# Kernel optimization log

Hardware: AMD Instinct MI355X
Metric: run time of the kernel (lower is better)

Reference implementation:

```python
import jax, jax.numpy as jnp
import numpy as np

B, S, E = 8, 2048, 1024
H, DK = 128, 8  # embed_dim = H * DK; DK = n_wires per quantum head


def setup_inputs() -> dict:
    key = jax.random.key(0)
    k1, k2, k3, k4 = jax.random.split(key, 4)
    x = jax.random.normal(k1, (B, S, E), dtype=jnp.float32)
    theta = jax.random.normal(k2, (H, DK), dtype=jnp.float32)  # trainable RX angles per head/wire
    W = jax.random.normal(k3, (E, E), dtype=jnp.float32) * (1.0 / np.sqrt(E))
    b = jax.random.normal(k4, (E,), dtype=jnp.float32) * 0.01
    return {"x": x, "theta": theta, "W": W, "b": b}


def reference(x, theta, W, b):
    # Quantum circuit per token/head: RX(x_i) then RX(theta_i) on wire i starting
    # from |0...0>. Single-qubit RX gates compose: RX(a)RX(b)=RX(a+b), and
    # <Z> after RX(angle)|0> = cos(angle). So the MeasureAll(PauliZ) output is
    # cos(x_i + theta_i) elementwise -- fully vectorized over batch/seq/head/wire.
    Bx, Sx, Ex = x.shape
    Hx, dk = theta.shape
    xs = x.reshape(Bx, Sx, Hx, dk)            # [B,S,H,dk]
    head_out = jnp.cos(xs + theta[None, None])  # [B,S,H,dk]
    out = head_out.reshape(Bx, Sx, Ex)
    return out @ W.T + b                       # combine Linear
```

## Files before the change

kernel.cpp:

```cpp
#include <hip/hip_runtime.h>
#include <hip/hip_bf16.h>
#include <stdint.h>

#define M_DIM 16384
#define N_DIM 1024
#define K_DIM 1024

typedef __attribute__((ext_vector_type(8))) short short8;
typedef __attribute__((ext_vector_type(4))) float f32x4;

#define GLD_LDS(g, l) __builtin_amdgcn_global_load_lds( \
    (const __attribute__((address_space(1))) unsigned int*)(g), \
    (__attribute__((address_space(3))) unsigned int*)(l), 16, 0, 0)

__device__ __forceinline__ unsigned short f2bf(float f) {
  union { float f; unsigned int u; } v;
  v.f = f;
  unsigned int u = v.u + 0x7FFFu + ((v.u >> 16) & 1u);
  return (unsigned short)(u >> 16);
}

#define PREP_A_BLOCKS (M_DIM * K_DIM / (256 * 8))
#define PREP_W_BLOCKS (N_DIM * K_DIM / (256 * 8))
__global__ __launch_bounds__(256) void prep_all(const float* __restrict__ x,
                                                const float* __restrict__ theta,
                                                const float* __restrict__ W,
                                                unsigned short* __restrict__ A,
                                                unsigned short* __restrict__ Wb) {
  if (blockIdx.x < PREP_A_BLOCKS) {
    const long i = ((long)blockIdx.x * 256 + threadIdx.x) * 8;
    const int k = (int)(i & (K_DIM - 1));
    float4 x0 = *(const float4*)(x + i);
    float4 x1 = *(const float4*)(x + i + 4);
    float4 t0 = *(const float4*)(theta + k);
    float4 t1 = *(const float4*)(theta + k + 4);
    union { unsigned short s[8]; short8 v; } o;
    o.s[0] = f2bf(__cosf(x0.x + t0.x));
    o.s[1] = f2bf(__cosf(x0.y + t0.y));
    o.s[2] = f2bf(__cosf(x0.z + t0.z));
    o.s[3] = f2bf(__cosf(x0.w + t0.w));
    o.s[4] = f2bf(__cosf(x1.x + t1.x));
    o.s[5] = f2bf(__cosf(x1.y + t1.y));
    o.s[6] = f2bf(__cosf(x1.z + t1.z));
    o.s[7] = f2bf(__cosf(x1.w + t1.w));
    *(short8*)(A + i) = o.v;
  } else {
    const long i = ((long)(blockIdx.x - PREP_A_BLOCKS) * 256 + threadIdx.x) * 8;
    float4 w0 = *(const float4*)(W + i);
    float4 w1 = *(const float4*)(W + i + 4);
    union { unsigned short s[8]; short8 v; } o;
    o.s[0] = f2bf(w0.x); o.s[1] = f2bf(w0.y); o.s[2] = f2bf(w0.z); o.s[3] = f2bf(w0.w);
    o.s[4] = f2bf(w1.x); o.s[5] = f2bf(w1.y); o.s[6] = f2bf(w1.z); o.s[7] = f2bf(w1.w);
    *(short8*)(Wb + i) = o.v;
  }
}

__global__ __launch_bounds__(512, 2) void gemm_bt(const unsigned short* __restrict__ A,
                                                  const unsigned short* __restrict__ Bt,
                                                  const float* __restrict__ bias,
                                                  float* __restrict__ C) {
  constexpr int BM = 256, BN = 256, BK = 64;
  constexpr int NT = K_DIM / BK;
  __shared__ unsigned short As[2 * BM * BK];
  __shared__ unsigned short Bs[2 * BN * BK];
  const int tid = threadIdx.x;

  const int L = blockIdx.y * 4 + blockIdx.x;
  const int xcd = L & 7;
  const int idx = L >> 3;
  const int by = xcd * 8 + (idx >> 2);
  const int bx = idx & 3;
  const int m0 = by * BM;
  const int n0 = bx * BN;

  const int lane = tid & 63;
  const int wave = tid >> 6;
  const int wm = (wave >> 2) * 128;
  const int wn = (wave & 3) * 64;
  const int fr = lane & 15;
  const int fq = lane >> 4;

  f32x4 acc[8][4] = {};

  const int csw = (tid & 7) ^ ((tid >> 3) & 7);
  const unsigned short* Ag = A + (long)(m0 + (tid >> 3)) * K_DIM + csw * 8;
  const unsigned short* Bg = Bt + (long)(n0 + (tid >> 3)) * K_DIM + csw * 8;
  unsigned short* Asd = As + tid * 8;
  unsigned short* Bsd = Bs + tid * 8;

#pragma unroll
  for (int i = 0; i < 4; ++i) GLD_LDS(Ag + (long)i * 64 * K_DIM, Asd + i * 4096);
#pragma unroll
  for (int i = 0; i < 4; ++i) GLD_LDS(Bg + (long)i * 64 * K_DIM, Bsd + i * 4096);
  Ag += BK;
  Bg += BK;

  for (int t = 0; t < NT; ++t) {
    const int cur = t & 1;
    if (t < NT - 1) {
      unsigned short* Ad = Asd + (cur ^ 1) * (BM * BK);
      unsigned short* Bd = Bsd + (cur ^ 1) * (BN * BK);
#pragma unroll
      for (int i = 0; i < 4; ++i) GLD_LDS(Ag + (long)i * 64 * K_DIM, Ad + i * 4096);
#pragma unroll
      for (int i = 0; i < 4; ++i) GLD_LDS(Bg + (long)i * 64 * K_DIM, Bd + i * 4096);
      Ag += BK;
      Bg += BK;
      asm volatile("s_waitcnt vmcnt(8)" ::: "memory");
    } else {
      asm volatile("s_waitcnt vmcnt(0)" ::: "memory");
    }
    __builtin_amdgcn_s_barrier();
    asm volatile("" ::: "memory");

    const unsigned short* SA = As + cur * (BM * BK);
    const unsigned short* SB = Bs + cur * (BN * BK);
#pragma unroll
    for (int ks = 0; ks < 2; ++ks) {
      const int swz = (((ks * 4 + fq) ^ (lane & 7)) * 8);
      short8 af[8], bf[4];
#pragma unroll
      for (int j = 0; j < 4; ++j)
        bf[j] = *(const short8*)(SB + (wn + j * 16 + fr) * BK + swz);
#pragma unroll
      for (int i = 0; i < 8; ++i)
        af[i] = *(const short8*)(SA + (wm + i * 16 + fr) * BK + swz);
      __builtin_amdgcn_s_setprio(1);
#pragma unroll
      for (int i = 0; i < 8; ++i)
#pragma unroll
        for (int j = 0; j < 4; ++j)
          acc[i][j] = __builtin_amdgcn_mfma_f32_16x16x32_bf16(af[i], bf[j], acc[i][j], 0, 0, 0);
      __builtin_amdgcn_s_setprio(0);
      if (ks == 0) {
        asm volatile("" ::: "memory");
        __builtin_amdgcn_s_barrier();
        asm volatile("" ::: "memory");
      }
    }
    asm volatile("" ::: "memory");
    __builtin_amdgcn_s_barrier();
    asm volatile("" ::: "memory");
  }

  const int cn = lane & 15;
  const int rq = (lane >> 4) * 4;
#pragma unroll
  for (int j = 0; j < 4; ++j) {
    const int n = n0 + wn + j * 16 + cn;
    const float bv = bias[n];
#pragma unroll
    for (int i = 0; i < 8; ++i) {
      const long mb = (long)(m0 + wm + i * 16 + rq) * N_DIM + n;
#pragma unroll
      for (int r = 0; r < 4; ++r)
        C[mb + (long)r * N_DIM] = acc[i][j][r] + bv;
    }
  }
}

extern "C" void kernel_launch(void* const* d_in, const int* in_sizes, int n_in,
                              void* d_out, int out_size, void* d_ws, size_t ws_size,
                              hipStream_t stream) {
  const float* x = (const float*)d_in[0];
  const float* theta = (const float*)d_in[1];
  const float* W = (const float*)d_in[2];
  const float* b = (const float*)d_in[3];
  float* out = (float*)d_out;

  unsigned short* Abf = (unsigned short*)d_ws;
  unsigned short* Wbf = Abf + (size_t)M_DIM * K_DIM;

  hipLaunchKernelGGL(prep_all, dim3(PREP_A_BLOCKS + PREP_W_BLOCKS), dim3(256), 0,
                     stream, x, theta, W, Abf, Wbf);
  hipLaunchKernelGGL(gemm_bt, dim3(N_DIM / 256, M_DIM / 256), dim3(512), 0, stream,
                     Abf, Wbf, b, out);
}
```

Baseline: 152.5 us.

## Restructure GEMM main loop into four-unit half-K LDS pipeline with phased MFMA

```diff
diff --git a/kernel.cpp b/kernel.cpp
--- a/kernel.cpp
+++ b/kernel.cpp
@@ -59,10 +59,9 @@
                                                   const unsigned short* __restrict__ Bt,
                                                   const float* __restrict__ bias,
                                                   float* __restrict__ C) {
-  constexpr int BM = 256, BN = 256, BK = 64;
-  constexpr int NT = K_DIM / BK;
-  __shared__ unsigned short As[2 * BM * BK];
-  __shared__ unsigned short Bs[2 * BN * BK];
+  constexpr int NTT = K_DIM / 64;
+  __shared__ unsigned short As[4 * 8192];
+  __shared__ unsigned short Bs[4 * 8192];
   const int tid = threadIdx.x;
 
   const int L = blockIdx.y * 4 + blockIdx.x;
@@ -70,8 +69,8 @@
   const int idx = L >> 3;
   const int by = xcd * 8 + (idx >> 2);
   const int bx = idx & 3;
-  const int m0 = by * BM;
-  const int n0 = bx * BN;
+  const int m0 = by * 256;
+  const int n0 = bx * 256;
 
   const int lane = tid & 63;
   const int wave = tid >> 6;
@@ -82,65 +81,123 @@
 
   f32x4 acc[8][4] = {};
 
-  const int csw = (tid & 7) ^ ((tid >> 3) & 7);
-  const unsigned short* Ag = A + (long)(m0 + (tid >> 3)) * K_DIM + csw * 8;
-  const unsigned short* Bg = Bt + (long)(n0 + (tid >> 3)) * K_DIM + csw * 8;
-  unsigned short* Asd = As + tid * 8;
-  unsigned short* Bsd = Bs + tid * 8;
-
-#pragma unroll
-  for (int i = 0; i < 4; ++i) GLD_LDS(Ag + (long)i * 64 * K_DIM, Asd + i * 4096);
-#pragma unroll
-  for (int i = 0; i < 4; ++i) GLD_LDS(Bg + (long)i * 64 * K_DIM, Bsd + i * 4096);
-  Ag += BK;
-  Bg += BK;
-
-  for (int t = 0; t < NT; ++t) {
-    const int cur = t & 1;
-    if (t < NT - 1) {
-      unsigned short* Ad = Asd + (cur ^ 1) * (BM * BK);
-      unsigned short* Bd = Bsd + (cur ^ 1) * (BN * BK);
-#pragma unroll
-      for (int i = 0; i < 4; ++i) GLD_LDS(Ag + (long)i * 64 * K_DIM, Ad + i * 4096);
-#pragma unroll
-      for (int i = 0; i < 4; ++i) GLD_LDS(Bg + (long)i * 64 * K_DIM, Bd + i * 4096);
-      Ag += BK;
-      Bg += BK;
-      asm volatile("s_waitcnt vmcnt(8)" ::: "memory");
-    } else {
-      asm volatile("s_waitcnt vmcnt(0)" ::: "memory");
-    }
-    __builtin_amdgcn_s_barrier();
-    asm volatile("" ::: "memory");
-
-    const unsigned short* SA = As + cur * (BM * BK);
-    const unsigned short* SB = Bs + cur * (BN * BK);
-#pragma unroll
-    for (int ks = 0; ks < 2; ++ks) {
-      const int swz = (((ks * 4 + fq) ^ (lane & 7)) * 8);
-      short8 af[8], bf[4];
-#pragma unroll
-      for (int j = 0; j < 4; ++j)
-        bf[j] = *(const short8*)(SB + (wn + j * 16 + fr) * BK + swz);
-#pragma unroll
-      for (int i = 0; i < 8; ++i)
-        af[i] = *(const short8*)(SA + (wm + i * 16 + fr) * BK + swz);
-      __builtin_amdgcn_s_setprio(1);
-#pragma unroll
-      for (int i = 0; i < 8; ++i)
-#pragma unroll
-        for (int j = 0; j < 4; ++j)
-          acc[i][j] = __builtin_amdgcn_mfma_f32_16x16x32_bf16(af[i], bf[j], acc[i][j], 0, 0, 0);
-      __builtin_amdgcn_s_setprio(0);
-      if (ks == 0) {
-        asm volatile("" ::: "memory");
-        __builtin_amdgcn_s_barrier();
-        asm volatile("" ::: "memory");
-      }
-    }
-    asm volatile("" ::: "memory");
-    __builtin_amdgcn_s_barrier();
-    asm volatile("" ::: "memory");
+  const int srow = ((tid >> 5) << 3) | (tid & 7);
+  const int kc = (tid >> 3) & 3;
+  const unsigned short* AgU = A + (long)(m0 + srow) * K_DIM + kc * 8;
+  const unsigned short* BgU = Bt + (long)(n0 + srow) * K_DIM + kc * 8;
+  unsigned short* AsD = As + tid * 8;
+  unsigned short* BsD = Bs + tid * 8;
+
+#define STAGE_A(UNIT, TAU, KH) do { \
+    const unsigned short* g_ = AgU + (TAU) * 64 + (KH) * 32; \
+    unsigned short* d_ = AsD + (UNIT) * 8192; \
+    GLD_LDS(g_, d_); \
+    GLD_LDS(g_ + (long)128 * K_DIM, d_ + 4096); \
+  } while (0)
+#define STAGE_B(UNIT, TAU, KH) do { \
+    const unsigned short* g_ = BgU + (TAU) * 64 + (KH) * 32; \
+    unsigned short* d_ = BsD + (UNIT) * 8192; \
+    GLD_LDS(g_, d_); \
+    GLD_LDS(g_ + (long)128 * K_DIM, d_ + 4096); \
+  } while (0)
+
+  const int baseA = ((wm >> 3) + (fr >> 3)) * 256 + fq * 64 + (fr & 7) * 8;
+  const int baseB = ((wn >> 3) + (fr >> 3)) * 256 + fq * 64 + (fr & 7) * 8;
+
+  short8 bf0, bf1, bf2, bf3;
+
+#define MFMA16(IH, A0, A1, A2, A3) do { \
+    __builtin_amdgcn_s_setprio(1); \
+    acc[(IH)*4+0][0] = __builtin_amdgcn_mfma_f32_16x16x32_bf16(A0, bf0, acc[(IH)*4+0][0], 0, 0, 0); \
+    acc[(IH)*4+0][1] = __builtin_amdgcn_mfma_f32_16x16x32_bf16(A0, bf1, acc[(IH)*4+0][1], 0, 0, 0); \
+    acc[(IH)*4+0][2] = __builtin_amdgcn_mfma_f32_16x16x32_bf16(A0, bf2, acc[(IH)*4+0][2], 0, 0, 0); \
+    acc[(IH)*4+0][3] = __builtin_amdgcn_mfma_f32_16x16x32_bf16(A0, bf3, acc[(IH)*4+0][3], 0, 0, 0); \
+    acc[(IH)*4+1][0] = __builtin_amdgcn_mfma_f32_16x16x32_bf16(A1, bf0, acc[(IH)*4+1][0], 0, 0, 0); \
+    acc[(IH)*4+1][1] = __builtin_amdgcn_mfma_f32_16x16x32_bf16(A1, bf1, acc[(IH)*4+1][1], 0, 0, 0); \
+    acc[(IH)*4+1][2] = __builtin_amdgcn_mfma_f32_16x16x32_bf16(A1, bf2, acc[(IH)*4+1][2], 0, 0, 0); \
+    acc[(IH)*4+1][3] = __builtin_amdgcn_mfma_f32_16x16x32_bf16(A1, bf3, acc[(IH)*4+1][3], 0, 0, 0); \
+    acc[(IH)*4+2][0] = __builtin_amdgcn_mfma_f32_16x16x32_bf16(A2, bf0, acc[(IH)*4+2][0], 0, 0, 0); \
+    acc[(IH)*4+2][1] = __builtin_amdgcn_mfma_f32_16x16x32_bf16(A2, bf1, acc[(IH)*4+2][1], 0, 0, 0); \
+    acc[(IH)*4+2][2] = __builtin_amdgcn_mfma_f32_16x16x32_bf16(A2, bf2, acc[(IH)*4+2][2], 0, 0, 0); \
+    acc[(IH)*4+2][3] = __builtin_amdgcn_mfma_f32_16x16x32_bf16(A2, bf3, acc[(IH)*4+2][3], 0, 0, 0); \
+    acc[(IH)*4+3][0] = __builtin_amdgcn_mfma_f32_16x16x32_bf16(A3, bf0, acc[(IH)*4+3][0], 0, 0, 0); \
+    acc[(IH)*4+3][1] = __builtin_amdgcn_mfma_f32_16x16x32_bf16(A3, bf1, acc[(IH)*4+3][1], 0, 0, 0); \
+    acc[(IH)*4+3][2] = __builtin_amdgcn_mfma_f32_16x16x32_bf16(A3, bf2, acc[(IH)*4+3][2], 0, 0, 0); \
+    acc[(IH)*4+3][3] = __builtin_amdgcn_mfma_f32_16x16x32_bf16(A3, bf3, acc[(IH)*4+3][3], 0, 0, 0); \
+    __builtin_amdgcn_s_setprio(0); \
+  } while (0)
+
+#define BAR() do { asm volatile("" ::: "memory"); __builtin_amdgcn_s_barrier(); \
+                   asm volatile("" ::: "memory"); } while (0)
+#define VMW(N) asm volatile("s_waitcnt vmcnt(" #N ")" ::: "memory")
+
+#define PHASE_LO(Au, Bu, ISSUE, WAIT) do { \
+    BAR(); \
+    ISSUE; \
+    bf0 = *(const short8*)((Bu) + baseB + 0); \
+    bf1 = *(const short8*)((Bu) + baseB + 512); \
+    bf2 = *(const short8*)((Bu) + baseB + 1024); \
+    bf3 = *(const short8*)((Bu) + baseB + 1536); \
+    { short8 a0 = *(const short8*)((Au) + baseA + 0); \
+      short8 a1 = *(const short8*)((Au) + baseA + 512); \
+      short8 a2 = *(const short8*)((Au) + baseA + 1024); \
+      short8 a3 = *(const short8*)((Au) + baseA + 1536); \
+      MFMA16(0, a0, a1, a2, a3); } \
+    WAIT; \
+  } while (0)
+
+#define PHASE_HI(Au, ISSUE, WAIT) do { \
+    BAR(); \
+    ISSUE; \
+    { short8 a0 = *(const short8*)((Au) + baseA + 2048); \
+      short8 a1 = *(const short8*)((Au) + baseA + 2560); \
+      short8 a2 = *(const short8*)((Au) + baseA + 3072); \
+      short8 a3 = *(const short8*)((Au) + baseA + 3584); \
+      MFMA16(1, a0, a1, a2, a3); } \
+    WAIT; \
+  } while (0)
+
+  STAGE_A(0, 0, 0);
+  STAGE_B(0, 0, 0);
+  STAGE_A(1, 0, 1);
+  STAGE_B(1, 0, 1);
+  STAGE_A(2, 1, 0);
+  STAGE_B(2, 1, 0);
+  VMW(8);
+
+  for (int t = 0; t < NTT - 2; ++t) {
+    const int db = t & 1;
+    const int u0 = db * 2;
+    const int u1 = db * 2 + 1;
+    const int v1 = (db ^ 1) * 2 + 1;
+    const unsigned short* Au0 = As + u0 * 8192;
+    const unsigned short* Bu0 = Bs + u0 * 8192;
+    const unsigned short* Au1 = As + u1 * 8192;
+    const unsigned short* Bu1 = Bs + u1 * 8192;
+    PHASE_LO(Au0, Bu0, STAGE_A(v1, t + 1, 1), (void)0);
+    PHASE_HI(Au0,      STAGE_B(v1, t + 1, 1), VMW(8));
+    PHASE_LO(Au1, Bu1, STAGE_A(u0, t + 2, 0), (void)0);
+    PHASE_HI(Au1,      STAGE_B(u0, t + 2, 0), VMW(8));
+  }
+  {
+    const unsigned short* Au0 = As;
+    const unsigned short* Bu0 = Bs;
+    const unsigned short* Au1 = As + 8192;
+    const unsigned short* Bu1 = Bs + 8192;
+    PHASE_LO(Au0, Bu0, STAGE_A(3, 15, 1), (void)0);
+    PHASE_HI(Au0,      STAGE_B(3, 15, 1), VMW(8));
+    PHASE_LO(Au1, Bu1, (void)0,           (void)0);
+    PHASE_HI(Au1,      (void)0,           VMW(4));
+  }
+  {
+    const unsigned short* Au0 = As + 2 * 8192;
+    const unsigned short* Bu0 = Bs + 2 * 8192;
+    const unsigned short* Au1 = As + 3 * 8192;
+    const unsigned short* Bu1 = Bs + 3 * 8192;
+    PHASE_LO(Au0, Bu0, (void)0, (void)0);
+    PHASE_HI(Au0,      (void)0, VMW(0));
+    PHASE_LO(Au1, Bu1, (void)0, (void)0);
+    PHASE_HI(Au1,      (void)0, (void)0);
   }
 
   const int cn = lane & 15;
```

Result: slower. 160.0 us (+4.9%).

## Fuse cosine activation and bf16 conversion into GEMM A-tile loading

Applied to the files above, without the earlier changes.

```diff
diff --git a/kernel.cpp b/kernel.cpp
--- a/kernel.cpp
+++ b/kernel.cpp
@@ -20,127 +20,131 @@
   return (unsigned short)(u >> 16);
 }
 
-#define PREP_A_BLOCKS (M_DIM * K_DIM / (256 * 8))
 #define PREP_W_BLOCKS (N_DIM * K_DIM / (256 * 8))
-__global__ __launch_bounds__(256) void prep_all(const float* __restrict__ x,
-                                                const float* __restrict__ theta,
-                                                const float* __restrict__ W,
-                                                unsigned short* __restrict__ A,
-                                                unsigned short* __restrict__ Wb) {
-  if (blockIdx.x < PREP_A_BLOCKS) {
-    const long i = ((long)blockIdx.x * 256 + threadIdx.x) * 8;
-    const int k = (int)(i & (K_DIM - 1));
-    float4 x0 = *(const float4*)(x + i);
-    float4 x1 = *(const float4*)(x + i + 4);
-    float4 t0 = *(const float4*)(theta + k);
-    float4 t1 = *(const float4*)(theta + k + 4);
-    union { unsigned short s[8]; short8 v; } o;
-    o.s[0] = f2bf(__cosf(x0.x + t0.x));
-    o.s[1] = f2bf(__cosf(x0.y + t0.y));
-    o.s[2] = f2bf(__cosf(x0.z + t0.z));
-    o.s[3] = f2bf(__cosf(x0.w + t0.w));
-    o.s[4] = f2bf(__cosf(x1.x + t1.x));
-    o.s[5] = f2bf(__cosf(x1.y + t1.y));
-    o.s[6] = f2bf(__cosf(x1.z + t1.z));
-    o.s[7] = f2bf(__cosf(x1.w + t1.w));
-    *(short8*)(A + i) = o.v;
-  } else {
-    const long i = ((long)(blockIdx.x - PREP_A_BLOCKS) * 256 + threadIdx.x) * 8;
-    float4 w0 = *(const float4*)(W + i);
-    float4 w1 = *(const float4*)(W + i + 4);
-    union { unsigned short s[8]; short8 v; } o;
-    o.s[0] = f2bf(w0.x); o.s[1] = f2bf(w0.y); o.s[2] = f2bf(w0.z); o.s[3] = f2bf(w0.w);
-    o.s[4] = f2bf(w1.x); o.s[5] = f2bf(w1.y); o.s[6] = f2bf(w1.z); o.s[7] = f2bf(w1.w);
-    *(short8*)(Wb + i) = o.v;
-  }
+__global__ __launch_bounds__(256) void prep_w(const float* __restrict__ W,
+                                              unsigned short* __restrict__ Wb) {
+  const long i = ((long)blockIdx.x * 256 + threadIdx.x) * 8;
+  float4 w0 = *(const float4*)(W + i);
+  float4 w1 = *(const float4*)(W + i + 4);
+  union { unsigned short s[8]; short8 v; } o;
+  o.s[0] = f2bf(w0.x); o.s[1] = f2bf(w0.y); o.s[2] = f2bf(w0.z); o.s[3] = f2bf(w0.w);
+  o.s[4] = f2bf(w1.x); o.s[5] = f2bf(w1.y); o.s[6] = f2bf(w1.z); o.s[7] = f2bf(w1.w);
+  *(short8*)(Wb + i) = o.v;
 }
 
-__global__ __launch_bounds__(512, 2) void gemm_bt(const unsigned short* __restrict__ A,
-                                                  const unsigned short* __restrict__ Bt,
-                                                  const float* __restrict__ bias,
-                                                  float* __restrict__ C) {
-  constexpr int BM = 256, BN = 256, BK = 64;
-  constexpr int NT = K_DIM / BK;
-  __shared__ unsigned short As[2 * BM * BK];
-  __shared__ unsigned short Bs[2 * BN * BK];
+__global__ __launch_bounds__(256, 2) void gemm_fused(const float* __restrict__ x,
+                                                     const float* __restrict__ theta,
+                                                     const unsigned short* __restrict__ Bt,
+                                                     const float* __restrict__ bias,
+                                                     float* __restrict__ C) {
+  constexpr int NTT = K_DIM / 64;
+  __shared__ unsigned short As[4 * 4096];
+  __shared__ unsigned short Bs[4 * 4096];
   const int tid = threadIdx.x;
 
-  const int L = blockIdx.y * 4 + blockIdx.x;
+  const int L = blockIdx.x;
   const int xcd = L & 7;
   const int idx = L >> 3;
-  const int by = xcd * 8 + (idx >> 2);
-  const int bx = idx & 3;
-  const int m0 = by * BM;
-  const int n0 = bx * BN;
+  const int by = xcd * 16 + (idx >> 3);
+  const int bx = idx & 7;
+  const int m0 = by * 128;
+  const int n0 = bx * 128;
 
   const int lane = tid & 63;
   const int wave = tid >> 6;
-  const int wm = (wave >> 2) * 128;
-  const int wn = (wave & 3) * 64;
+  const int wm = (wave >> 1) * 64;
+  const int wn = (wave & 1) * 64;
   const int fr = lane & 15;
   const int fq = lane >> 4;
 
-  f32x4 acc[8][4] = {};
+  f32x4 acc[4][4] = {};
 
-  const int csw = (tid & 7) ^ ((tid >> 3) & 7);
-  const unsigned short* Ag = A + (long)(m0 + (tid >> 3)) * K_DIM + csw * 8;
-  const unsigned short* Bg = Bt + (long)(n0 + (tid >> 3)) * K_DIM + csw * 8;
-  unsigned short* Asd = As + tid * 8;
-  unsigned short* Bsd = Bs + tid * 8;
+  const int srow = ((tid >> 5) << 3) | (tid & 7);
+  const int kc = (tid >> 3) & 3;
+  const float* xg = x + (long)(m0 + srow) * K_DIM + kc * 8;
+  const unsigned short* Bg = Bt + (long)(n0 + srow) * K_DIM + kc * 8;
+  unsigned short* BsD = Bs + tid * 8;
 
-#pragma unroll
-  for (int i = 0; i < 4; ++i) GLD_LDS(Ag + (long)i * 64 * K_DIM, Asd + i * 4096);
-#pragma unroll
-  for (int i = 0; i < 4; ++i) GLD_LDS(Bg + (long)i * 64 * K_DIM, Bsd + i * 4096);
-  Ag += BK;
-  Bg += BK;
+  float4 xa[4][2];
+  float4 th[2][2];
 
-  for (int t = 0; t < NT; ++t) {
-    const int cur = t & 1;
-    if (t < NT - 1) {
-      unsigned short* Ad = Asd + (cur ^ 1) * (BM * BK);
-      unsigned short* Bd = Bsd + (cur ^ 1) * (BN * BK);
-#pragma unroll
-      for (int i = 0; i < 4; ++i) GLD_LDS(Ag + (long)i * 64 * K_DIM, Ad + i * 4096);
-#pragma unroll
-      for (int i = 0; i < 4; ++i) GLD_LDS(Bg + (long)i * 64 * K_DIM, Bd + i * 4096);
-      Ag += BK;
-      Bg += BK;
-      asm volatile("s_waitcnt vmcnt(8)" ::: "memory");
-    } else {
-      asm volatile("s_waitcnt vmcnt(0)" ::: "memory");
+#define LOADA(T) do { \
+    _Pragma("unroll") \
+    for (int kh = 0; kh < 2; ++kh) { \
+      th[kh][0] = *(const float4*)(theta + (T) * 64 + kh * 32 + kc * 8); \
+      th[kh][1] = *(const float4*)(theta + (T) * 64 + kh * 32 + kc * 8 + 4); \
+      _Pragma("unroll") \
+      for (int i2 = 0; i2 < 2; ++i2) { \
+        const float* g_ = xg + (long)i2 * 64 * K_DIM + (T) * 64 + kh * 32; \
+        xa[kh * 2 + i2][0] = *(const float4*)(g_); \
+        xa[kh * 2 + i2][1] = *(const float4*)(g_ + 4); \
+      } \
+    } \
+  } while (0)
+
+#define STAGEB(P, T) do { \
+    _Pragma("unroll") \
+    for (int kh = 0; kh < 2; ++kh) \
+      _Pragma("unroll") \
+      for (int i2 = 0; i2 < 2; ++i2) \
+        GLD_LDS(Bg + (long)i2 * 64 * K_DIM + (T) * 64 + kh * 32, \
+                BsD + ((P) * 2 + kh) * 4096 + i2 * 2048); \
+  } while (0)
+
+#define WRITEA(P) do { \
+    _Pragma("unroll") \
+    for (int kh = 0; kh < 2; ++kh) \
+      _Pragma("unroll") \
+      for (int i2 = 0; i2 < 2; ++i2) { \
+        union { unsigned short s[8]; short8 v; } o; \
+        o.s[0] = f2bf(__cosf(xa[kh * 2 + i2][0].x + th[kh][0].x)); \
+        o.s[1] = f2bf(__cosf(xa[kh * 2 + i2][0].y + th[kh][0].y)); \
+        o.s[2] = f2bf(__cosf(xa[kh * 2 + i2][0].z + th[kh][0].z)); \
+        o.s[3] = f2bf(__cosf(xa[kh * 2 + i2][0].w + th[kh][0].w)); \
+        o.s[4] = f2bf(__cosf(xa[kh * 2 + i2][1].x + th[kh][1].x)); \
+        o.s[5] = f2bf(__cosf(xa[kh * 2 + i2][1].y + th[kh][1].y)); \
+        o.s[6] = f2bf(__cosf(xa[kh * 2 + i2][1].z + th[kh][1].z)); \
+        o.s[7] = f2bf(__cosf(xa[kh * 2 + i2][1].w + th[kh][1].w)); \
+        *(short8*)(As + ((P) * 2 + kh) * 4096 + i2 * 2048 + tid * 8) = o.v; \
+      } \
+  } while (0)
+
+  const int baseA = ((wm >> 3) + (fr >> 3)) * 256 + fq * 64 + (fr & 7) * 8;
+  const int baseB = ((wn >> 3) + (fr >> 3)) * 256 + fq * 64 + (fr & 7) * 8;
+
+#define COMPUTE(P) do { \
+    _Pragma("unroll") \
+    for (int kh = 0; kh < 2; ++kh) { \
+      const unsigned short* Au = As + ((P) * 2 + kh) * 4096; \
+      const unsigned short* Bu = Bs + ((P) * 2 + kh) * 4096; \
+      short8 af[4], bfv[4]; \
+      _Pragma("unroll") \
+      for (int j = 0; j < 4; ++j) bfv[j] = *(const short8*)(Bu + baseB + j * 512); \
+      _Pragma("unroll") \
+      for (int i = 0; i < 4; ++i) af[i] = *(const short8*)(Au + baseA + i * 512); \
+      _Pragma("unroll") \
+      for (int i = 0; i < 4; ++i) \
+        _Pragma("unroll") \
+        for (int j = 0; j < 4; ++j) \
+          acc[i][j] = __builtin_amdgcn_mfma_f32_16x16x32_bf16(af[i], bfv[j], acc[i][j], 0, 0, 0); \
+    } \
+  } while (0)
+
+#define VMW0() asm volatile("s_waitcnt vmcnt(0)" ::: "memory")
+
+  LOADA(0);
+  STAGEB(0, 0);
+
+  for (int t = 0; t < NTT; ++t) {
+    const int p = t & 1;
+    VMW0();
+    WRITEA(p);
+    __syncthreads();
+    if (t < NTT - 1) {
+      STAGEB(p ^ 1, t + 1);
+      LOADA(t + 1);
     }
-    __builtin_amdgcn_s_barrier();
-    asm volatile("" ::: "memory");
-
-    const unsigned short* SA = As + cur * (BM * BK);
-    const unsigned short* SB = Bs + cur * (BN * BK);
-#pragma unroll
-    for (int ks = 0; ks < 2; ++ks) {
-      const int swz = (((ks * 4 + fq) ^ (lane & 7)) * 8);
-      short8 af[8], bf[4];
-#pragma unroll
-      for (int j = 0; j < 4; ++j)
-        bf[j] = *(const short8*)(SB + (wn + j * 16 + fr) * BK + swz);
-#pragma unroll
-      for (int i = 0; i < 8; ++i)
-        af[i] = *(const short8*)(SA + (wm + i * 16 + fr) * BK + swz);
-      __builtin_amdgcn_s_setprio(1);
-#pragma unroll
-      for (int i = 0; i < 8; ++i)
-#pragma unroll
-        for (int j = 0; j < 4; ++j)
-          acc[i][j] = __builtin_amdgcn_mfma_f32_16x16x32_bf16(af[i], bf[j], acc[i][j], 0, 0, 0);
-      __builtin_amdgcn_s_setprio(0);
-      if (ks == 0) {
-        asm volatile("" ::: "memory");
-        __builtin_amdgcn_s_barrier();
-        asm volatile("" ::: "memory");
-      }
-    }
-    asm volatile("" ::: "memory");
-    __builtin_amdgcn_s_barrier();
-    asm volatile("" ::: "memory");
+    COMPUTE(p);
   }
 
   const int cn = lane & 15;
@@ -150,7 +154,7 @@
     const int n = n0 + wn + j * 16 + cn;
     const float bv = bias[n];
 #pragma unroll
-    for (int i = 0; i < 8; ++i) {
+    for (int i = 0; i < 4; ++i) {
       const long mb = (long)(m0 + wm + i * 16 + rq) * N_DIM + n;
 #pragma unroll
       for (int r = 0; r < 4; ++r)
@@ -168,11 +172,9 @@
   const float* b = (const float*)d_in[3];
   float* out = (float*)d_out;
 
-  unsigned short* Abf = (unsigned short*)d_ws;
-  unsigned short* Wbf = Abf + (size_t)M_DIM * K_DIM;
+  unsigned short* Wbf = (unsigned short*)d_ws;
 
-  hipLaunchKernelGGL(prep_all, dim3(PREP_A_BLOCKS + PREP_W_BLOCKS), dim3(256), 0,
-                     stream, x, theta, W, Abf, Wbf);
-  hipLaunchKernelGGL(gemm_bt, dim3(N_DIM / 256, M_DIM / 256), dim3(512), 0, stream,
-                     Abf, Wbf, b, out);
+  hipLaunchKernelGGL(prep_w, dim3(PREP_W_BLOCKS), dim3(256), 0, stream, W, Wbf);
+  hipLaunchKernelGGL(gemm_fused, dim3(M_DIM / 128 * (N_DIM / 128)), dim3(256), 0,
+                     stream, x, theta, Wbf, b, out);
 }
```

New measurement: 212.5 us. +39.4%, slower.
